# Performance work log

Hardware: AMD Instinct MI355X
Metric: run time of the kernel (lower is better)

The kernel has to match this reference:

```python
import jax, jax.numpy as jnp
import numpy as np

N_NODES = 50000
N_EDGES = 800000
N_GRAPHS = 256
N_FEAT, N_HID, N_EMB = 128, 256, 256
BN_EPS = 1e-5
W_SCALE = 0.05  # keep activations well-scaled through 3 layers


def setup_inputs() -> dict:
    key = jax.random.key(0)
    ks = jax.random.split(key, 9)
    x = jax.random.normal(ks[0], (N_NODES, N_FEAT), jnp.float32)
    edge_index = jax.random.randint(ks[1], (2, N_EDGES), 0, N_NODES)
    batch = jnp.sort(jax.random.randint(ks[2], (N_NODES,), 0, N_GRAPHS))
    return {
        "x": x,
        "edge_index": edge_index,
        "batch": batch,
        "W1_0": jax.random.normal(ks[3], (N_FEAT, N_HID), jnp.float32) * W_SCALE,
        "W2_0": jax.random.normal(ks[4], (N_HID, N_HID), jnp.float32) * W_SCALE,
        "gamma0": jnp.ones((N_HID,), jnp.float32),
        "beta0": jnp.zeros((N_HID,), jnp.float32),
        "W1_1": jax.random.normal(ks[5], (N_HID, N_HID), jnp.float32) * W_SCALE,
        "W2_1": jax.random.normal(ks[6], (N_HID, N_HID), jnp.float32) * W_SCALE,
        "gamma1": jnp.ones((N_HID,), jnp.float32),
        "beta1": jnp.zeros((N_HID,), jnp.float32),
        "W1_2": jax.random.normal(ks[7], (N_HID, N_HID), jnp.float32) * W_SCALE,
        "W2_2": jax.random.normal(ks[8], (N_HID, N_EMB), jnp.float32) * W_SCALE,
    }


def _gin_conv(x, src, dst, W1, W2):
    # PyG GINConv, eps=0: nn((1+eps)*x_i + sum_{j in N(i)} x_j)
    agg = jax.ops.segment_sum(x[src], dst, num_segments=N_NODES)  # [N, d]
    h = x + agg
    return jax.nn.relu(h @ W1) @ W2  # Linear(bias=False) -> act -> Linear(bias=False)


def _batch_norm(h, gamma, beta):
    # BatchNorm1d in training mode: biased batch stats over nodes
    mean = jnp.mean(h, axis=0)
    var = jnp.var(h, axis=0)
    return (h - mean) * jax.lax.rsqrt(var + BN_EPS) * gamma + beta


def reference(x, edge_index, batch, W1_0, W2_0, gamma0, beta0,
              W1_1, W2_1, gamma1, beta1, W1_2, W2_2):
    src, dst = edge_index[0], edge_index[1]
    layers = [(W1_0, W2_0, gamma0, beta0), (W1_1, W2_1, gamma1, beta1)]
    xs = []
    h = x
    for W1, W2, g, b in layers:  # n_layers-1 conv+act+BN blocks
        h = jax.nn.relu(_gin_conv(h, src, dst, W1, W2))
        h = _batch_norm(h, g, b)
        xs.append(h)
    h = _gin_conv(h, src, dst, W1_2, W2_2)  # final conv: no act, no BN
    xs.append(h)
    xpool = jax.ops.segment_sum(h, batch, num_segments=N_GRAPHS)  # global_add_pool
    return xpool, jnp.concatenate(xs, axis=1)
```

## Files before the change

kernel.cpp:

```cpp
#include <hip/hip_runtime.h>
#include <stdint.h>

typedef unsigned int u32;
typedef unsigned short u16;

using s16x8 = __attribute__((ext_vector_type(8))) short;
using f32x4 = __attribute__((ext_vector_type(4))) float;

#define N_NODES_C 50000
#define N_EDGES_C 800000
#define N_GRAPHS_C 256
#define N_FEAT_C 128
#define N_HID_C 256

static __device__ __forceinline__ float bf2f(u16 u) {
  union { u32 u; float f; } c; c.u = ((u32)u) << 16; return c.f;
}
static __device__ __forceinline__ u16 f2bf(float f) {
  union { float f; u32 u; } c; c.f = f;
  u32 u = c.u;
  return (u16)((u + 0x7fffu + ((u >> 16) & 1u)) >> 16);
}

static __device__ __forceinline__ void gload_lds16(const u16* g, u16* l) {
  __builtin_amdgcn_global_load_lds(
      (const __attribute__((address_space(1))) unsigned int*)g,
      (__attribute__((address_space(3))) unsigned int*)l, 16, 0, 0);
}

__global__ void convt_all_kernel(const float* __restrict__ Wa, const float* __restrict__ Wb,
                                 const float* __restrict__ Wc, const float* __restrict__ Wd,
                                 const float* __restrict__ We, const float* __restrict__ Wf,
                                 u16* oa, u16* ob, u16* oc, u16* od, u16* oe, u16* of_,
                                 int* cnt, int* flags, float* stats0, float* stats1) {
  int m = blockIdx.y;
  if (m == 6) {
    int idx = blockIdx.x * 256 + threadIdx.x;
    if (idx <= N_NODES_C) cnt[idx] = 0;
    if (idx < 64) flags[idx] = 0;
    if (idx < 512) { stats0[idx] = 0.f; stats1[idx] = 0.f; }
    return;
  }
  const float* W; u16* o; int K;
  switch (m) {
    case 0: W = Wa; o = oa; K = 128; break;
    case 1: W = Wb; o = ob; K = 256; break;
    case 2: W = Wc; o = oc; K = 256; break;
    case 3: W = Wd; o = od; K = 256; break;
    case 4: W = We; o = oe; K = 256; break;
    default: W = Wf; o = of_; K = 256; break;
  }
  int idx = blockIdx.x * 256 + threadIdx.x;
  if (idx >= K * 256) return;
  int n = idx / K, k = idx - n * K;
  o[idx] = f2bf(W[(size_t)k * 256 + n]);
}

__global__ void cvt4_kernel(const float* __restrict__ x, u16* __restrict__ xb, int n4) {
  int idx = blockIdx.x * 256 + threadIdx.x;
  if (idx >= n4) return;
  float4 v = reinterpret_cast<const float4*>(x)[idx];
  u32 lo = (u32)f2bf(v.x) | ((u32)f2bf(v.y) << 16);
  u32 hi = (u32)f2bf(v.z) | ((u32)f2bf(v.w) << 16);
  uint2 w; w.x = lo; w.y = hi;
  reinterpret_cast<uint2*>(xb)[idx] = w;
}

__global__ void count_kernel(const int* __restrict__ dst, int* __restrict__ cnt, int E) {
  int e = blockIdx.x * 256 + threadIdx.x;
  if (e < E) atomicAdd(&cnt[dst[e]], 1);
}

__global__ void scan_fused_kernel(const int* __restrict__ cnt, int* __restrict__ offs,
                                  int* __restrict__ cursor, int* __restrict__ flags, int n) {
  __shared__ int sd[1024];
  __shared__ int prefix_sh;
  int b = blockIdx.x;
  int i = b * 1024 + (int)threadIdx.x;
  int v = (i < n) ? cnt[i] : 0;
  sd[threadIdx.x] = v;
  __syncthreads();
  for (int off = 1; off < 1024; off <<= 1) {
    int t = ((int)threadIdx.x >= off) ? sd[threadIdx.x - off] : 0;
    __syncthreads();
    sd[threadIdx.x] += t;
    __syncthreads();
  }
  if (threadIdx.x == 0) {
    int total = sd[1023];
    atomicExch(&flags[b], (total << 1) | 1);
    int p = 0;
    for (int j = 0; j < b; j++) {
      int f;
      do { f = atomicAdd(&flags[j], 0); } while (!(f & 1));
      p += (f >> 1);
    }
    prefix_sh = p;
  }
  __syncthreads();
  int excl = sd[threadIdx.x] - v + prefix_sh;
  if (i < n) { offs[i] = excl; cursor[i] = excl; }
  if (i == n) offs[n] = N_EDGES_C;
}

__global__ void fill_kernel(const int* __restrict__ src, const int* __restrict__ dst,
                            int* __restrict__ cursor, int* __restrict__ csr, int E) {
  int e = blockIdx.x * 256 + threadIdx.x;
  if (e < E) {
    int p = atomicAdd(&cursor[dst[e]], 1);
    csr[p] = src[e];
  }
}

template <int D, bool AFFINE>
__global__ __launch_bounds__(256) void agg_kernel(const u16* __restrict__ xin,
                                                  const int* __restrict__ offs,
                                                  const int* __restrict__ csr,
                                                  const float* __restrict__ sb,
                                                  float* __restrict__ concat_prev,
                                                  u16* __restrict__ hout) {
  constexpr int LPE = D / 8;
  constexpr int EPW = 64 / LPE;
  int wid = threadIdx.x >> 6, lane = threadIdx.x & 63;
  int node = blockIdx.x * 4 + wid;
  if (node >= N_NODES_C) return;
  int sub = lane / LPE;
  int fl = lane % LPE;
  int f0 = fl * 8;
  float acc[8], own[8];
  if (sub == 0) {
    uint4 v = *reinterpret_cast<const uint4*>(xin + (size_t)node * D + f0);
    const u32* pv = reinterpret_cast<const u32*>(&v);
#pragma unroll
    for (int t = 0; t < 4; t++) {
      acc[2 * t] = bf2f((u16)pv[t]);
      acc[2 * t + 1] = bf2f((u16)(pv[t] >> 16));
      own[2 * t] = acc[2 * t];
      own[2 * t + 1] = acc[2 * t + 1];
    }
  } else {
#pragma unroll
    for (int t = 0; t < 8; t++) acc[t] = 0.f;
  }
  int e0 = offs[node];
  int e1 = offs[node + 1];
  int e = e0 + sub;
  if (EPW == 2) {
    for (; e + 3 * EPW < e1; e += 4 * EPW) {
      int s0 = csr[e], s1 = csr[e + EPW], s2 = csr[e + 2 * EPW], s3 = csr[e + 3 * EPW];
      uint4 v0 = *reinterpret_cast<const uint4*>(xin + (size_t)s0 * D + f0);
      uint4 v1 = *reinterpret_cast<const uint4*>(xin + (size_t)s1 * D + f0);
      uint4 v2 = *reinterpret_cast<const uint4*>(xin + (size_t)s2 * D + f0);
      uint4 v3 = *reinterpret_cast<const uint4*>(xin + (size_t)s3 * D + f0);
      const u32* p0 = reinterpret_cast<const u32*>(&v0);
      const u32* p1 = reinterpret_cast<const u32*>(&v1);
      const u32* p2 = reinterpret_cast<const u32*>(&v2);
      const u32* p3 = reinterpret_cast<const u32*>(&v3);
#pragma unroll
      for (int t = 0; t < 4; t++) {
        acc[2 * t] += (bf2f((u16)p0[t]) + bf2f((u16)p1[t])) +
                      (bf2f((u16)p2[t]) + bf2f((u16)p3[t]));
        acc[2 * t + 1] += (bf2f((u16)(p0[t] >> 16)) + bf2f((u16)(p1[t] >> 16))) +
                          (bf2f((u16)(p2[t] >> 16)) + bf2f((u16)(p3[t] >> 16)));
      }
    }
  } else {
    for (; e + EPW < e1; e += 2 * EPW) {
      int s0 = csr[e], s1 = csr[e + EPW];
      uint4 v0 = *reinterpret_cast<const uint4*>(xin + (size_t)s0 * D + f0);
      uint4 v1 = *reinterpret_cast<const uint4*>(xin + (size_t)s1 * D + f0);
      const u32* p0 = reinterpret_cast<const u32*>(&v0);
      const u32* p1 = reinterpret_cast<const u32*>(&v1);
#pragma unroll
      for (int t = 0; t < 4; t++) {
        acc[2 * t] += bf2f((u16)p0[t]) + bf2f((u16)p1[t]);
        acc[2 * t + 1] += bf2f((u16)(p0[t] >> 16)) + bf2f((u16)(p1[t] >> 16));
      }
    }
  }
  for (; e < e1; e += EPW) {
    int s = csr[e];
    uint4 v = *reinterpret_cast<const uint4*>(xin + (size_t)s * D + f0);
    const u32* pv = reinterpret_cast<const u32*>(&v);
#pragma unroll
    for (int t = 0; t < 4; t++) {
      acc[2 * t] += bf2f((u16)pv[t]);
      acc[2 * t + 1] += bf2f((u16)(pv[t] >> 16));
    }
  }
#pragma unroll
  for (int j = 0; j < 8; j++) {
    if (EPW == 4) acc[j] += __shfl_xor(acc[j], 16, 64);
    acc[j] += __shfl_xor(acc[j], 32, 64);
  }
  if (sub == 0) {
    if (AFFINE) {
      float4 sca = *reinterpret_cast<const float4*>(sb + f0);
      float4 scb = *reinterpret_cast<const float4*>(sb + f0 + 4);
      float4 bia = *reinterpret_cast<const float4*>(sb + 256 + f0);
      float4 bib = *reinterpret_cast<const float4*>(sb + 256 + f0 + 4);
      float sc[8] = {sca.x, sca.y, sca.z, sca.w, scb.x, scb.y, scb.z, scb.w};
      float bi[8] = {bia.x, bia.y, bia.z, bia.w, bib.x, bib.y, bib.z, bib.w};
      float4 y0, y1;
      y0.x = fmaf(own[0], sc[0], bi[0]); y0.y = fmaf(own[1], sc[1], bi[1]);
      y0.z = fmaf(own[2], sc[2], bi[2]); y0.w = fmaf(own[3], sc[3], bi[3]);
      y1.x = fmaf(own[4], sc[4], bi[4]); y1.y = fmaf(own[5], sc[5], bi[5]);
      y1.z = fmaf(own[6], sc[6], bi[6]); y1.w = fmaf(own[7], sc[7], bi[7]);
      *reinterpret_cast<float4*>(concat_prev + (size_t)node * 768 + f0) = y0;
      *reinterpret_cast<float4*>(concat_prev + (size_t)node * 768 + f0 + 4) = y1;
      float dp1 = (float)(e1 - e0 + 1);
#pragma unroll
      for (int j = 0; j < 8; j++) acc[j] = fmaf(acc[j], sc[j], bi[j] * dp1);
    }
    u32 w[4];
#pragma unroll
    for (int t = 0; t < 4; t++)
      w[t] = (u32)f2bf(acc[2 * t]) | ((u32)f2bf(acc[2 * t + 1]) << 16);
    *reinterpret_cast<uint4*>(hout + (size_t)node * D + f0) =
        *reinterpret_cast<const uint4*>(w);
  }
}

template <int K, bool RELU, bool OUTF32, bool STATS>
__global__ __launch_bounds__(512, 2) void gemm_kernel(const u16* __restrict__ A,
                                                      const u16* __restrict__ Bt,
                                                      u16* __restrict__ outB,
                                                      float* __restrict__ outF, int ldc,
                                                      float* __restrict__ statsp) {
  constexpr int BM = 128, BK = 64;
  __shared__ u16 Al[BM * BK];
  __shared__ u16 Bl[256 * BK];
  const int tid = threadIdx.x;
  const int wid = tid >> 6, lane = tid & 63;
  const int brow = blockIdx.x * BM;
  const int wr = (wid >> 2) * 64;
  const int wc = (wid & 3) * 64;
  f32x4 acc[4][4] = {};

  const int lrow = lane >> 3;
  const int lw = lane & 7;
  const int colA = (lw ^ lrow) * 8;
  const int sw = (lane & 7) << 3;

  for (int k0 = 0; k0 < K; k0 += BK) {
#pragma unroll
    for (int i = 0; i < 6; i++) {
      int c = wid * 6 + i;
      if (c < 16) {
        int r = c * 8 + lrow;
        int gr = brow + r;
        gr = gr < N_NODES_C ? gr : N_NODES_C - 1;
        gload_lds16(A + (size_t)gr * K + k0 + colA, &Al[c * 512]);
      } else {
        int cc = c - 16;
        int r = cc * 8 + lrow;
        gload_lds16(Bt + (size_t)r * K + k0 + colA, &Bl[cc * 512]);
      }
    }
    __syncthreads();
#pragma unroll
    for (int ks = 0; ks < BK; ks += 32) {
      const int kk = ks + (lane >> 4) * 8;
      const int ki = kk ^ sw;
      s16x8 a[4], b[4];
#pragma unroll
      for (int m = 0; m < 4; m++)
        a[m] = *reinterpret_cast<const s16x8*>(&Al[(wr + m * 16 + (lane & 15)) * 64 + ki]);
#pragma unroll
      for (int n = 0; n < 4; n++)
        b[n] = *reinterpret_cast<const s16x8*>(&Bl[(wc + n * 16 + (lane & 15)) * 64 + ki]);
#pragma unroll
      for (int m = 0; m < 4; m++)
#pragma unroll
        for (int n = 0; n < 4; n++)
          acc[m][n] = __builtin_amdgcn_mfma_f32_16x16x32_bf16(a[m], b[n], acc[m][n], 0, 0, 0);
    }
    __syncthreads();
  }

  const int cb = wc + (lane & 15);
  const int rsub = (lane >> 4) * 4;
  float s1[4] = {0.f, 0.f, 0.f, 0.f}, s2[4] = {0.f, 0.f, 0.f, 0.f};
#pragma unroll
  for (int m = 0; m < 4; m++) {
#pragma unroll
    for (int r = 0; r < 4; r++) {
      int row = brow + wr + m * 16 + rsub + r;
      if (row >= N_NODES_C) continue;
#pragma unroll
      for (int n = 0; n < 4; n++) {
        float v = acc[m][n][r];
        if (RELU) v = v > 0.f ? v : 0.f;
        int col = cb + n * 16;
        if (OUTF32)
          outF[(size_t)row * ldc + col] = v;
        else
          outB[(size_t)row * ldc + col] = f2bf(v);
        if (STATS) { s1[n] += v; s2[n] += v * v; }
      }
    }
  }
  if (STATS) {
#pragma unroll
    for (int n = 0; n < 4; n++) {
      float a0 = s1[n], b0 = s2[n];
      a0 += __shfl_xor(a0, 16, 64);
      b0 += __shfl_xor(b0, 16, 64);
      a0 += __shfl_xor(a0, 32, 64);
      b0 += __shfl_xor(b0, 32, 64);
      if (lane < 16) {
        atomicAdd(&statsp[cb + n * 16], a0);
        atomicAdd(&statsp[256 + cb + n * 16], b0);
      }
    }
  }
}

__global__ void scalebias_kernel(const float* __restrict__ stats, const float* __restrict__ gamma,
                                 const float* __restrict__ beta, float* __restrict__ sb) {
  int f = threadIdx.x;
  const float invM = 1.0f / (float)N_NODES_C;
  float mean = stats[f] * invM;
  float var = stats[256 + f] * invM - mean * mean;
  float sc = gamma[f] * rsqrtf(var + 1e-5f);
  sb[f] = sc;
  sb[256 + f] = beta[f] - mean * sc;
}

__global__ __launch_bounds__(256) void pool_kernel(const float* __restrict__ c, int ldc,
                                                   const int* __restrict__ batch,
                                                   float* __restrict__ outp) {
  __shared__ float red[1024];
  int g = blockIdx.x;
  int wid = threadIdx.x >> 6, lane = threadIdx.x & 63;
  int lo = 0, hi = N_NODES_C;
  while (lo < hi) { int mid = (lo + hi) >> 1; if (batch[mid] < g) lo = mid + 1; else hi = mid; }
  int start = lo;
  hi = N_NODES_C;
  while (lo < hi) { int mid = (lo + hi) >> 1; if (batch[mid] <= g) lo = mid + 1; else hi = mid; }
  int end = lo;
  float acc[4] = {0.f, 0.f, 0.f, 0.f};
  for (int r = start + wid; r < end; r += 4) {
    float4 v = *reinterpret_cast<const float4*>(c + (size_t)r * ldc + lane * 4);
    acc[0] += v.x; acc[1] += v.y; acc[2] += v.z; acc[3] += v.w;
  }
#pragma unroll
  for (int j = 0; j < 4; j++) red[wid * 256 + lane * 4 + j] = acc[j];
  __syncthreads();
  int f = threadIdx.x;
  float s = red[f] + red[256 + f] + red[512 + f] + red[768 + f];
  outp[(size_t)g * 256 + f] = s;
}

extern "C" void kernel_launch(void* const* d_in, const int* in_sizes, int n_in,
                              void* d_out, int out_size, void* d_ws, size_t ws_size,
                              hipStream_t stream) {
  (void)in_sizes; (void)n_in; (void)out_size; (void)ws_size;
  const float* x = (const float*)d_in[0];
  const int* ei = (const int*)d_in[1];
  const int* batch = (const int*)d_in[2];
  const float* W1_0 = (const float*)d_in[3];
  const float* W2_0 = (const float*)d_in[4];
  const float* gamma0 = (const float*)d_in[5];
  const float* beta0 = (const float*)d_in[6];
  const float* W1_1 = (const float*)d_in[7];
  const float* W2_1 = (const float*)d_in[8];
  const float* gamma1 = (const float*)d_in[9];
  const float* beta1 = (const float*)d_in[10];
  const float* W1_2 = (const float*)d_in[11];
  const float* W2_2 = (const float*)d_in[12];

  float* out = (float*)d_out;
  float* xpool = out;
  float* concat = out + (size_t)N_GRAPHS_C * N_HID_C;

  char* ws = (char*)d_ws;
  size_t off = 0;
  auto alloc = [&](size_t bytes) -> char* {
    char* p = ws + off;
    off = (off + bytes + 255) & ~(size_t)255;
    return p;
  };
  int* cnt = (int*)alloc((N_NODES_C + 1) * 4);
  int* offs = (int*)alloc((N_NODES_C + 1) * 4);
  int* cursor = (int*)alloc(N_NODES_C * 4);
  int* flags = (int*)alloc(64 * 4);
  int* csr = (int*)alloc((size_t)N_EDGES_C * 4);
  u16* xb = (u16*)alloc((size_t)N_NODES_C * N_FEAT_C * 2);
  u16* hin = (u16*)alloc((size_t)N_NODES_C * N_HID_C * 2);
  u16* tbuf = (u16*)alloc((size_t)N_NODES_C * N_HID_C * 2);
  u16* hpre = (u16*)alloc((size_t)N_NODES_C * N_HID_C * 2);
  u16* w10t = (u16*)alloc((size_t)N_FEAT_C * N_HID_C * 2);
  u16* w20t = (u16*)alloc((size_t)N_HID_C * N_HID_C * 2);
  u16* w11t = (u16*)alloc((size_t)N_HID_C * N_HID_C * 2);
  u16* w21t = (u16*)alloc((size_t)N_HID_C * N_HID_C * 2);
  u16* w12t = (u16*)alloc((size_t)N_HID_C * N_HID_C * 2);
  u16* w22t = (u16*)alloc((size_t)N_HID_C * N_HID_C * 2);
  float* stats0 = (float*)alloc(512 * 4);
  float* stats1 = (float*)alloc(512 * 4);
  float* sb0 = (float*)alloc(512 * 4);
  float* sb1 = (float*)alloc(512 * 4);

  const int* srcv = ei;
  const int* dstv = ei + N_EDGES_C;
  const int nb = (N_NODES_C + 1023) / 1024;
  const int ggrid = (N_NODES_C + 127) / 128;

  convt_all_kernel<<<dim3(256, 7), 256, 0, stream>>>(
      W1_0, W2_0, W1_1, W2_1, W1_2, W2_2, w10t, w20t, w11t, w21t, w12t, w22t,
      cnt, flags, stats0, stats1);
  cvt4_kernel<<<(N_NODES_C * N_FEAT_C / 4 + 255) / 256, 256, 0, stream>>>(
      x, xb, N_NODES_C * N_FEAT_C / 4);

  count_kernel<<<(N_EDGES_C + 255) / 256, 256, 0, stream>>>(dstv, cnt, N_EDGES_C);
  scan_fused_kernel<<<nb, 1024, 0, stream>>>(cnt, offs, cursor, flags, N_NODES_C);
  fill_kernel<<<(N_EDGES_C + 255) / 256, 256, 0, stream>>>(srcv, dstv, cursor, csr, N_EDGES_C);

  agg_kernel<128, false><<<(N_NODES_C + 3) / 4, 256, 0, stream>>>(
      xb, offs, csr, nullptr, nullptr, hin);
  gemm_kernel<128, true, false, false><<<ggrid, 512, 0, stream>>>(
      hin, w10t, tbuf, nullptr, N_HID_C, nullptr);
  gemm_kernel<256, true, false, true><<<ggrid, 512, 0, stream>>>(
      tbuf, w20t, hpre, nullptr, N_HID_C, stats0);
  scalebias_kernel<<<1, 256, 0, stream>>>(stats0, gamma0, beta0, sb0);

  agg_kernel<256, true><<<(N_NODES_C + 3) / 4, 256, 0, stream>>>(
      hpre, offs, csr, sb0, concat + 0, hin);
  gemm_kernel<256, true, false, false><<<ggrid, 512, 0, stream>>>(
      hin, w11t, tbuf, nullptr, N_HID_C, nullptr);
  gemm_kernel<256, true, false, true><<<ggrid, 512, 0, stream>>>(
      tbuf, w21t, hpre, nullptr, N_HID_C, stats1);
  scalebias_kernel<<<1, 256, 0, stream>>>(stats1, gamma1, beta1, sb1);

  agg_kernel<256, true><<<(N_NODES_C + 3) / 4, 256, 0, stream>>>(
      hpre, offs, csr, sb1, concat + 256, hin);
  gemm_kernel<256, true, false, false><<<ggrid, 512, 0, stream>>>(
      hin, w12t, tbuf, nullptr, N_HID_C, nullptr);
  gemm_kernel<256, false, true, false><<<ggrid, 512, 0, stream>>>(
      tbuf, w22t, nullptr, concat + 512, 768, nullptr);

  pool_kernel<<<N_GRAPHS_C, 256, 0, stream>>>(concat + 512, 768, batch, xpool);
}
```

Before: 445.9 us.

## Fuse BN scale/bias and pooling into GEMM epilogues, merge convert and count

Merges the x bf16 conversion and degree counting into one 2D-grid launch. The BN scale/bias computation moves into the stats GEMM via a last-block completion counter. Global add pooling moves into the final GEMM epilogue using per-element float atomics into xpool, which is zeroed in the init kernel. This removes several small launches and the pool pass over the output, at the cost of heavy, contended atomic traffic on a small pooled buffer.

```diff
diff --git a/kernel.cpp b/kernel.cpp
--- a/kernel.cpp
+++ b/kernel.cpp
@@ -32,13 +32,16 @@
                                  const float* __restrict__ Wc, const float* __restrict__ Wd,
                                  const float* __restrict__ We, const float* __restrict__ Wf,
                                  u16* oa, u16* ob, u16* oc, u16* od, u16* oe, u16* of_,
-                                 int* cnt, int* flags, float* stats0, float* stats1) {
+                                 int* cnt, int* flags, int* donecnt,
+                                 float* stats0, float* stats1, float* xpool) {
   int m = blockIdx.y;
   if (m == 6) {
     int idx = blockIdx.x * 256 + threadIdx.x;
     if (idx <= N_NODES_C) cnt[idx] = 0;
     if (idx < 64) flags[idx] = 0;
+    if (idx < 2) donecnt[idx] = 0;
     if (idx < 512) { stats0[idx] = 0.f; stats1[idx] = 0.f; }
+    if (idx < N_GRAPHS_C * N_HID_C) xpool[idx] = 0.f;
     return;
   }
   const float* W; u16* o; int K;
@@ -56,19 +59,19 @@
   o[idx] = f2bf(W[(size_t)k * 256 + n]);
 }
 
-__global__ void cvt4_kernel(const float* __restrict__ x, u16* __restrict__ xb, int n4) {
+__global__ void cvt_count_kernel(const float* __restrict__ x, u16* __restrict__ xb, int n4,
+                                 const int* __restrict__ dst, int* __restrict__ cnt, int E) {
   int idx = blockIdx.x * 256 + threadIdx.x;
-  if (idx >= n4) return;
-  float4 v = reinterpret_cast<const float4*>(x)[idx];
-  u32 lo = (u32)f2bf(v.x) | ((u32)f2bf(v.y) << 16);
-  u32 hi = (u32)f2bf(v.z) | ((u32)f2bf(v.w) << 16);
-  uint2 w; w.x = lo; w.y = hi;
-  reinterpret_cast<uint2*>(xb)[idx] = w;
-}
-
-__global__ void count_kernel(const int* __restrict__ dst, int* __restrict__ cnt, int E) {
-  int e = blockIdx.x * 256 + threadIdx.x;
-  if (e < E) atomicAdd(&cnt[dst[e]], 1);
+  if (blockIdx.y == 0) {
+    if (idx >= n4) return;
+    float4 v = reinterpret_cast<const float4*>(x)[idx];
+    u32 lo = (u32)f2bf(v.x) | ((u32)f2bf(v.y) << 16);
+    u32 hi = (u32)f2bf(v.z) | ((u32)f2bf(v.w) << 16);
+    uint2 w; w.x = lo; w.y = hi;
+    reinterpret_cast<uint2*>(xb)[idx] = w;
+  } else {
+    if (idx < E) atomicAdd(&cnt[dst[idx]], 1);
+  }
 }
 
 __global__ void scan_fused_kernel(const int* __restrict__ cnt, int* __restrict__ offs,
@@ -221,15 +224,18 @@
   }
 }
 
-template <int K, bool RELU, bool OUTF32, bool STATS>
-__global__ __launch_bounds__(512, 2) void gemm_kernel(const u16* __restrict__ A,
-                                                      const u16* __restrict__ Bt,
-                                                      u16* __restrict__ outB,
-                                                      float* __restrict__ outF, int ldc,
-                                                      float* __restrict__ statsp) {
+template <int K, bool RELU, bool OUTF32, bool STATS, bool POOL>
+__global__ __launch_bounds__(512, 2) void gemm_kernel(
+    const u16* __restrict__ A, const u16* __restrict__ Bt,
+    u16* __restrict__ outB, float* __restrict__ outF, int ldc,
+    float* __restrict__ statsp, const float* __restrict__ gamma,
+    const float* __restrict__ beta, float* __restrict__ sbout,
+    int* __restrict__ donecnt, const int* __restrict__ batch,
+    float* __restrict__ xpool) {
   constexpr int BM = 128, BK = 64;
   __shared__ u16 Al[BM * BK];
   __shared__ u16 Bl[256 * BK];
+  __shared__ int amlast;
   const int tid = threadIdx.x;
   const int wid = tid >> 6, lane = tid & 63;
   const int brow = blockIdx.x * BM;
@@ -287,6 +293,8 @@
     for (int r = 0; r < 4; r++) {
       int row = brow + wr + m * 16 + rsub + r;
       if (row >= N_NODES_C) continue;
+      int bg = 0;
+      if (POOL) bg = batch[row];
 #pragma unroll
       for (int n = 0; n < 4; n++) {
         float v = acc[m][n][r];
@@ -297,6 +305,7 @@
         else
           outB[(size_t)row * ldc + col] = f2bf(v);
         if (STATS) { s1[n] += v; s2[n] += v * v; }
+        if (POOL) atomicAdd(&xpool[(size_t)bg * 256 + col], v);
       }
     }
   }
@@ -313,43 +322,21 @@
         atomicAdd(&statsp[256 + cb + n * 16], b0);
       }
     }
-  }
-}
-
-__global__ void scalebias_kernel(const float* __restrict__ stats, const float* __restrict__ gamma,
-                                 const float* __restrict__ beta, float* __restrict__ sb) {
-  int f = threadIdx.x;
-  const float invM = 1.0f / (float)N_NODES_C;
-  float mean = stats[f] * invM;
-  float var = stats[256 + f] * invM - mean * mean;
-  float sc = gamma[f] * rsqrtf(var + 1e-5f);
-  sb[f] = sc;
-  sb[256 + f] = beta[f] - mean * sc;
-}
-
-__global__ __launch_bounds__(256) void pool_kernel(const float* __restrict__ c, int ldc,
-                                                   const int* __restrict__ batch,
-                                                   float* __restrict__ outp) {
-  __shared__ float red[1024];
-  int g = blockIdx.x;
-  int wid = threadIdx.x >> 6, lane = threadIdx.x & 63;
-  int lo = 0, hi = N_NODES_C;
-  while (lo < hi) { int mid = (lo + hi) >> 1; if (batch[mid] < g) lo = mid + 1; else hi = mid; }
-  int start = lo;
-  hi = N_NODES_C;
-  while (lo < hi) { int mid = (lo + hi) >> 1; if (batch[mid] <= g) lo = mid + 1; else hi = mid; }
-  int end = lo;
-  float acc[4] = {0.f, 0.f, 0.f, 0.f};
-  for (int r = start + wid; r < end; r += 4) {
-    float4 v = *reinterpret_cast<const float4*>(c + (size_t)r * ldc + lane * 4);
-    acc[0] += v.x; acc[1] += v.y; acc[2] += v.z; acc[3] += v.w;
-  }
-#pragma unroll
-  for (int j = 0; j < 4; j++) red[wid * 256 + lane * 4 + j] = acc[j];
-  __syncthreads();
-  int f = threadIdx.x;
-  float s = red[f] + red[256 + f] + red[512 + f] + red[768 + f];
-  outp[(size_t)g * 256 + f] = s;
+    __threadfence();
+    if (tid == 0) amlast = (atomicAdd(donecnt, 1) == (int)gridDim.x - 1) ? 1 : 0;
+    __syncthreads();
+    if (amlast && tid < 256) {
+      int f = tid;
+      const float invM = 1.0f / (float)N_NODES_C;
+      float s = atomicAdd(&statsp[f], 0.0f);
+      float sq = atomicAdd(&statsp[256 + f], 0.0f);
+      float mean = s * invM;
+      float var = sq * invM - mean * mean;
+      float sc = gamma[f] * rsqrtf(var + 1e-5f);
+      sbout[f] = sc;
+      sbout[256 + f] = beta[f] - mean * sc;
+    }
+  }
 }
 
 extern "C" void kernel_launch(void* const* d_in, const int* in_sizes, int n_in,
@@ -385,6 +372,7 @@
   int* offs = (int*)alloc((N_NODES_C + 1) * 4);
   int* cursor = (int*)alloc(N_NODES_C * 4);
   int* flags = (int*)alloc(64 * 4);
+  int* donecnt = (int*)alloc(2 * 4);
   int* csr = (int*)alloc((size_t)N_EDGES_C * 4);
   u16* xb = (u16*)alloc((size_t)N_NODES_C * N_FEAT_C * 2);
   u16* hin = (u16*)alloc((size_t)N_NODES_C * N_HID_C * 2);
@@ -405,39 +393,41 @@
   const int* dstv = ei + N_EDGES_C;
   const int nb = (N_NODES_C + 1023) / 1024;
   const int ggrid = (N_NODES_C + 127) / 128;
+  const int n4 = N_NODES_C * N_FEAT_C / 4;
 
   convt_all_kernel<<<dim3(256, 7), 256, 0, stream>>>(
       W1_0, W2_0, W1_1, W2_1, W1_2, W2_2, w10t, w20t, w11t, w21t, w12t, w22t,
-      cnt, flags, stats0, stats1);
-  cvt4_kernel<<<(N_NODES_C * N_FEAT_C / 4 + 255) / 256, 256, 0, stream>>>(
-      x, xb, N_NODES_C * N_FEAT_C / 4);
-
-  count_kernel<<<(N_EDGES_C + 255) / 256, 256, 0, stream>>>(dstv, cnt, N_EDGES_C);
+      cnt, flags, donecnt, stats0, stats1, xpool);
+  cvt_count_kernel<<<dim3((n4 + 255) / 256, 2), 256, 0, stream>>>(
+      x, xb, n4, dstv, cnt, N_EDGES_C);
+
   scan_fused_kernel<<<nb, 1024, 0, stream>>>(cnt, offs, cursor, flags, N_NODES_C);
   fill_kernel<<<(N_EDGES_C + 255) / 256, 256, 0, stream>>>(srcv, dstv, cursor, csr, N_EDGES_C);
 
   agg_kernel<128, false><<<(N_NODES_C + 3) / 4, 256, 0, stream>>>(
       xb, offs, csr, nullptr, nullptr, hin);
-  gemm_kernel<128, true, false, false><<<ggrid, 512, 0, stream>>>(
-      hin, w10t, tbuf, nullptr, N_HID_C, nullptr);
-  gemm_kernel<256, true, false, true><<<ggrid, 512, 0, stream>>>(
-      tbuf, w20t, hpre, nullptr, N_HID_C, stats0);
-  scalebias_kernel<<<1, 256, 0, stream>>>(stats0, gamma0, beta0, sb0);
+  gemm_kernel<128, true, false, false, false><<<ggrid, 512, 0, stream>>>(
+      hin, w10t, tbuf, nullptr, N_HID_C, nullptr, nullptr, nullptr, nullptr, nullptr,
+      nullptr, nullptr);
+  gemm_kernel<256, true, false, true, false><<<ggrid, 512, 0, stream>>>(
+      tbuf, w20t, hpre, nullptr, N_HID_C, stats0, gamma0, beta0, sb0, donecnt,
+      nullptr, nullptr);
 
   agg_kernel<256, true><<<(N_NODES_C + 3) / 4, 256, 0, stream>>>(
       hpre, offs, csr, sb0, concat + 0, hin);
-  gemm_kernel<256, true, false, false><<<ggrid, 512, 0, stream>>>(
-      hin, w11t, tbuf, nullptr, N_HID_C, nullptr);
-  gemm_kernel<256, true, false, true><<<ggrid, 512, 0, stream>>>(
-      tbuf, w21t, hpre, nullptr, N_HID_C, stats1);
-  scalebias_kernel<<<1, 256, 0, stream>>>(stats1, gamma1, beta1, sb1);
+  gemm_kernel<256, true, false, false, false><<<ggrid, 512, 0, stream>>>(
+      hin, w11t, tbuf, nullptr, N_HID_C, nullptr, nullptr, nullptr, nullptr, nullptr,
+      nullptr, nullptr);
+  gemm_kernel<256, true, false, true, false><<<ggrid, 512, 0, stream>>>(
+      tbuf, w21t, hpre, nullptr, N_HID_C, stats1, gamma1, beta1, sb1, donecnt + 1,
+      nullptr, nullptr);
 
   agg_kernel<256, true><<<(N_NODES_C + 3) / 4, 256, 0, stream>>>(
       hpre, offs, csr, sb1, concat + 256, hin);
-  gemm_kernel<256, true, false, false><<<ggrid, 512, 0, stream>>>(
-      hin, w12t, tbuf, nullptr, N_HID_C, nullptr);
-  gemm_kernel<256, false, true, false><<<ggrid, 512, 0, stream>>>(
-      tbuf, w22t, nullptr, concat + 512, 768, nullptr);
-
-  pool_kernel<<<N_GRAPHS_C, 256, 0, stream>>>(concat + 512, 768, batch, xpool);
-}
+  gemm_kernel<256, true, false, false, false><<<ggrid, 512, 0, stream>>>(
+      hin, w12t, tbuf, nullptr, N_HID_C, nullptr, nullptr, nullptr, nullptr, nullptr,
+      nullptr, nullptr);
+  gemm_kernel<256, false, true, false, true><<<ggrid, 512, 0, stream>>>(
+      tbuf, w22t, nullptr, concat + 512, 768, nullptr, nullptr, nullptr, nullptr, nullptr,
+      batch, xpool);
+}
```

New measurement: 715.3 us. 60.4% more time.
